# Kernel tuning notes

Hardware: AMD Instinct MI355X
Metric: run time of the kernel (lower is better)

The kernel has to match this reference:

```python
import jax, jax.numpy as jnp
import numpy as np

N_NODES = 100000
D = 128


def setup_inputs() -> dict:
    key = jax.random.key(0)
    ks = jax.random.split(key, 6)
    x = jax.random.normal(ks[0], (N_NODES, 300), dtype=jnp.float32)
    n_id = jnp.arange(N_NODES, dtype=jnp.int64)
    edge_index = jax.random.randint(ks[1], (2, 1600000), 0, N_NODES, dtype=jnp.int64)
    history = jax.random.randint(ks[2], (4096, 50), 0, N_NODES, dtype=jnp.int64)
    candidates = jax.random.randint(ks[3], (4096, 20), 0, N_NODES, dtype=jnp.int64)
    W_enc = jax.random.normal(ks[4], (300, D), dtype=jnp.float32) * 0.05
    W_gnn = jax.random.normal(ks[5], (D, D), dtype=jnp.float32) * 0.05
    return {"x": x, "n_id": n_id, "edge_index": edge_index,
            "history": history, "candidates": candidates,
            "W_enc": W_enc, "W_gnn": W_gnn}


def reference(x, n_id, edge_index, history, candidates, W_enc, W_gnn):
    N = x.shape[0]
    # news encoder: linear projection of raw node features -> [N, D]
    news_emb = x @ W_enc
    # gnn: mean aggregation over incoming edges, then linear
    src, dst = edge_index[0], edge_index[1]
    agg = jax.ops.segment_sum(news_emb[src], dst, num_segments=N)      # [N, D]
    deg = jax.ops.segment_sum(jnp.ones((src.shape[0], 1), news_emb.dtype), dst,
                              num_segments=N)                          # [N, 1]
    struct_emb = (agg / jnp.maximum(deg, 1.0)) @ W_gnn
    xx = news_emb + struct_emb                                          # [N, D]
    # scatter into dense lookup table (n_id == arange -> max_id == N, static)
    news_lookup = jnp.zeros((N, xx.shape[1]), xx.dtype).at[n_id].set(xx)
    # gather histories / candidates
    history_embs = news_lookup[history]                                 # [B, H, D]
    cand_embs = news_lookup[candidates]                                 # [B, C, D]
    mask = (history != 0).astype(xx.dtype)                              # [B, H]
    sum_embs = jnp.einsum('bhd,bh->bd', history_embs, mask)
    num_read = jnp.clip(mask.sum(axis=1, keepdims=True), 1e-9, None)
    user_vec = sum_embs / num_read                                      # [B, D]
    scores = jnp.einsum('bcd,bd->bc', cand_embs, user_vec)              # [B, C]
    return scores
```

## Files before the change

### kernel.cpp

```cpp
#include <hip/hip_runtime.h>

#define NN 100000
#define DD 128
#define KE 300
#define NE 1600000
#define NB 4096
#define HL 50
#define CL 20

#define NBUCK 1563
#define SLOT  1280
#define PBLK  250
#define EPB   6400
#define EPT   25
#define EBLK  1563
#define ENCB  512

#define WTE_N 40960
#define WTG_N 16384
#define PREPB ((WTE_N + WTG_N + 255) / 256)

typedef unsigned short ushort_t;
typedef unsigned char uchar_t;
using bf16x8 = __attribute__((ext_vector_type(8))) short;
using f32x4  = __attribute__((ext_vector_type(4))) float;
using v2f    = __attribute__((ext_vector_type(2))) float;

union U4B { uint4 u; bf16x8 b; unsigned a[4]; };

__device__ __forceinline__ ushort_t f2bf(float f) {
    unsigned u = __float_as_uint(f);
    unsigned r = u + 0x7FFF + ((u >> 16) & 1);
    return (ushort_t)(r >> 16);
}
__device__ __forceinline__ float bf2f(unsigned s) {
    return __uint_as_float(s << 16);
}
__device__ __forceinline__ bf16x8 pack8(float4 a, float4 b) {
    U4B r;
    r.a[0] = (unsigned)f2bf(a.x) | ((unsigned)f2bf(a.y) << 16);
    r.a[1] = (unsigned)f2bf(a.z) | ((unsigned)f2bf(a.w) << 16);
    r.a[2] = (unsigned)f2bf(b.x) | ((unsigned)f2bf(b.y) << 16);
    r.a[3] = (unsigned)f2bf(b.z) | ((unsigned)f2bf(b.w) << 16);
    return r.b;
}

__device__ __forceinline__ bf16x8 loadA8m(const float* __restrict__ x,
                                          int row, int col, bool rowok) {
    float v[8];
#pragma unroll
    for (int j = 0; j < 8; ++j) {
        int c = col + j;
        v[j] = (rowok && c < KE) ? x[(long long)row * KE + c] : 0.f;
    }
    return pack8(make_float4(v[0], v[1], v[2], v[3]),
                 make_float4(v[4], v[5], v[6], v[7]));
}

__global__ __launch_bounds__(256) void k_prep(const int* __restrict__ ei,
                                              unsigned* __restrict__ gcur,
                                              unsigned* __restrict__ pairs,
                                              const float* __restrict__ We,
                                              const float* __restrict__ Wg,
                                              ushort_t* __restrict__ wte,
                                              ushort_t* __restrict__ wtg) {
    __shared__ unsigned sh[NBUCK], sb[NBUCK], sc[NBUCK];
    const int tid = threadIdx.x;

    if (blockIdx.x < PBLK) {
        const int eb = blockIdx.x * EPB;
        for (int i = tid; i < NBUCK; i += 256) sh[i] = 0;
        __syncthreads();

        unsigned val[EPT], bk[EPT];
#pragma unroll
        for (int l = 0; l < EPT; ++l) {
            int e = eb + l * 256 + tid;
            unsigned src = (unsigned)ei[e];
            unsigned dst = (unsigned)ei[NE + e];
            val[l] = (src << 6) | (dst & 63u);
            bk[l] = dst >> 6;
            atomicAdd(&sh[bk[l]], 1u);
        }
        __syncthreads();

        for (int i = tid; i < NBUCK; i += 256) {
            unsigned h = sh[i];
            sb[i] = (unsigned)i * SLOT + (h ? atomicAdd(&gcur[i], h) : 0u);
            sc[i] = 0;
        }
        __syncthreads();

#pragma unroll
        for (int l = 0; l < EPT; ++l) {
            unsigned b = bk[l];
            unsigned pos = sb[b] + atomicAdd(&sc[b], 1u);
            if (pos < (b + 1u) * SLOT) pairs[pos] = val[l];
        }
        return;
    }

    int i = (blockIdx.x - PBLK) * 256 + tid;
    if (i < WTE_N) {
        int j = i & 7, lane = (i >> 3) & 63, cf = (i >> 9) & 7, ch = i >> 12;
        int k = ch * 32 + (lane >> 4) * 8 + j;
        int n = cf * 16 + (lane & 15);
        wte[i] = f2bf((k < KE) ? We[k * DD + n] : 0.f);
    } else if (i < WTE_N + WTG_N) {
        int t = i - WTE_N;
        int j = t & 7, lane = (t >> 3) & 63, cf = (t >> 9) & 7, ks = t >> 12;
        int k = ks * 32 + (lane >> 4) * 8 + j;
        int n = cf * 16 + (lane & 15);
        wtg[t] = f2bf(Wg[k * DD + n]);
    }
}

__global__ __launch_bounds__(256, 1) void enc_mfma(const float* __restrict__ x,
                                                   const ushort_t* __restrict__ wtF,
                                                   ushort_t* __restrict__ news,
                                                   uchar_t* __restrict__ nf8) {
    __shared__ uchar_t f8s[64 * DD];
    const int tid = threadIdx.x;
    const int w = tid >> 6, lane = tid & 63;
    const int hl = lane & 15, kg = lane >> 4;

    bf16x8 B[10][8];
#pragma unroll
    for (int c = 0; c < 10; ++c)
#pragma unroll
        for (int cf = 0; cf < 8; ++cf)
            B[c][cf] = *(const bf16x8*)&wtF[(c * 8 + cf) * 512 + lane * 8];

    for (int tile = blockIdx.x; tile < EBLK; tile += gridDim.x) {
        const int row0 = tile * 64 + w * 16;
        const int r0 = row0 + hl;
        const bool ok0 = r0 < NN;
        const float* xr = &x[(long long)r0 * KE + kg * 8];
        const float4 fz = make_float4(0.f, 0.f, 0.f, 0.f);

        float4 ra[9][2];
        if (ok0) {
#pragma unroll
            for (int c = 0; c < 9; ++c) {
                const float4* p = (const float4*)(xr + c * 32);
                ra[c][0] = p[0];
                ra[c][1] = p[1];
            }
        } else {
#pragma unroll
            for (int c = 0; c < 9; ++c) { ra[c][0] = fz; ra[c][1] = fz; }
        }
        bf16x8 a9 = loadA8m(x, r0, 288 + kg * 8, ok0);

        f32x4 acc[8];
#pragma unroll
        for (int j = 0; j < 8; ++j) acc[j] = (f32x4)0.f;

#pragma unroll
        for (int c = 0; c < 9; ++c) {
            bf16x8 a = pack8(ra[c][0], ra[c][1]);
#pragma unroll
            for (int cf = 0; cf < 8; ++cf)
                acc[cf] = __builtin_amdgcn_mfma_f32_16x16x32_bf16(a, B[c][cf], acc[cf], 0, 0, 0);
        }
#pragma unroll
        for (int cf = 0; cf < 8; ++cf)
            acc[cf] = __builtin_amdgcn_mfma_f32_16x16x32_bf16(a9, B[9][cf], acc[cf], 0, 0, 0);

#pragma unroll
        for (int cf = 0; cf < 8; ++cf)
#pragma unroll
            for (int j = 0; j < 4; ++j) {
                int lr = w * 16 + kg * 4 + j;
                int grow = tile * 64 + lr;
                int gcol = cf * 16 + hl;
                if (grow < NN)
                    news[(long long)grow * DD + gcol] = f2bf(acc[cf][j]);
                int p = __builtin_amdgcn_cvt_pk_fp8_f32(acc[cf][j], 0.f, 0, false);
                f8s[lr * DD + gcol] = (uchar_t)(p & 0xFF);
            }
        __syncthreads();
        {
            int r = tid >> 2, boff = (tid & 3) * 32;
            int grow = tile * 64 + r;
            if (grow < NN) {
                const uint4* s = (const uint4*)&f8s[r * DD + boff];
                uint4* d = (uint4*)&nf8[(long long)grow * DD + boff];
                d[0] = s[0];
                d[1] = s[1];
            }
        }
        __syncthreads();
    }
}

__global__ __launch_bounds__(512) void k_baggnn(const unsigned* __restrict__ gcur,
                                                const unsigned* __restrict__ pairs,
                                                const uchar_t* __restrict__ nf8,
                                                const ushort_t* __restrict__ news,
                                                const ushort_t* __restrict__ wtF,
                                                ushort_t* __restrict__ xxb) {
    __shared__ unsigned srcs[SLOT];
    __shared__ unsigned hist[64], base[64], cur[64];
    __shared__ ushort_t aggs[64 * DD];
    const int tid = threadIdx.x;
    const int b = blockIdx.x;
    int cnt = (int)gcur[b];
    if (cnt > SLOT) cnt = SLOT;

    if (tid < 64) hist[tid] = 0;
    __syncthreads();
    for (int i = tid; i < cnt; i += 512)
        atomicAdd(&hist[pairs[b * SLOT + i] & 63u], 1u);
    __syncthreads();

    if (tid < 64) {
        unsigned h = hist[tid], v = h;
#pragma unroll
        for (int off = 1; off < 64; off <<= 1) {
            unsigned n = __shfl_up(v, off);
            if (tid >= off) v += n;
        }
        base[tid] = v - h;
        cur[tid]  = v - h;
    }
    __syncthreads();

    for (int i = tid; i < cnt; i += 512) {
        unsigned v = pairs[b * SLOT + i];
        srcs[atomicAdd(&cur[v & 63u], 1u)] = v >> 6;
    }
    __syncthreads();

    const int w = tid >> 6, lane = tid & 63;
    const int e = lane >> 4, l = lane & 15;
    for (int d = w; d < 64; d += 8) {
        int gd = b * 64 + d;
        if (gd >= NN) break;
        int s0 = (int)base[d], c = (int)hist[d];
        float acc[8];
#pragma unroll
        for (int j = 0; j < 8; ++j) acc[j] = 0.f;

        uint2 v = make_uint2(0u, 0u);
        if (e < c)
            v = *(const uint2*)&nf8[(long long)srcs[s0 + e] * DD + l * 8];
        for (int i = 4; i < c; i += 4) {
            uint2 vn = make_uint2(0u, 0u);
            int ii = i + e;
            if (ii < c)
                vn = *(const uint2*)&nf8[(long long)srcs[s0 + ii] * DD + l * 8];
            v2f d0 = __builtin_amdgcn_cvt_pk_f32_fp8((int)v.x, false);
            v2f d1 = __builtin_amdgcn_cvt_pk_f32_fp8((int)v.x, true);
            acc[0] += d0[0]; acc[1] += d0[1]; acc[2] += d1[0]; acc[3] += d1[1];
            d0 = __builtin_amdgcn_cvt_pk_f32_fp8((int)v.y, false);
            d1 = __builtin_amdgcn_cvt_pk_f32_fp8((int)v.y, true);
            acc[4] += d0[0]; acc[5] += d0[1]; acc[6] += d1[0]; acc[7] += d1[1];
            v = vn;
        }
        {
            v2f d0 = __builtin_amdgcn_cvt_pk_f32_fp8((int)v.x, false);
            v2f d1 = __builtin_amdgcn_cvt_pk_f32_fp8((int)v.x, true);
            acc[0] += d0[0]; acc[1] += d0[1]; acc[2] += d1[0]; acc[3] += d1[1];
            d0 = __builtin_amdgcn_cvt_pk_f32_fp8((int)v.y, false);
            d1 = __builtin_amdgcn_cvt_pk_f32_fp8((int)v.y, true);
            acc[4] += d0[0]; acc[5] += d0[1]; acc[6] += d1[0]; acc[7] += d1[1];
        }

#pragma unroll
        for (int j = 0; j < 8; ++j) {
            acc[j] += __shfl_xor(acc[j], 16);
            acc[j] += __shfl_xor(acc[j], 32);
        }
        if (e == 0) {
            uint4 o;
            o.x = (unsigned)f2bf(acc[0]) | ((unsigned)f2bf(acc[1]) << 16);
            o.y = (unsigned)f2bf(acc[2]) | ((unsigned)f2bf(acc[3]) << 16);
            o.z = (unsigned)f2bf(acc[4]) | ((unsigned)f2bf(acc[5]) << 16);
            o.w = (unsigned)f2bf(acc[6]) | ((unsigned)f2bf(acc[7]) << 16);
            *(uint4*)&aggs[d * DD + (l ^ (d & 15)) * 8] = o;
        }
    }
    __syncthreads();

    const int hl = lane & 15, kg = lane >> 4;
    const int rw = (w & 3) * 16;
    const int cfb = (w >> 2) * 4;
    U4B a[4];
#pragma unroll
    for (int ks = 0; ks < 4; ++ks)
        a[ks].u = *(const uint4*)&aggs[(rw + hl) * DD + ((ks * 4 + kg) ^ hl) * 8];

    f32x4 acc[4];
#pragma unroll
    for (int j = 0; j < 4; ++j) acc[j] = (f32x4)0.f;

#pragma unroll
    for (int ks = 0; ks < 4; ++ks) {
        const ushort_t* bp = &wtF[(ks * 8 + cfb) * 512 + lane * 8];
#pragma unroll
        for (int cf = 0; cf < 4; ++cf) {
            bf16x8 bfr = *(const bf16x8*)&bp[cf * 512];
            acc[cf] = __builtin_amdgcn_mfma_f32_16x16x32_bf16(a[ks].b, bfr, acc[cf], 0, 0, 0);
        }
    }

#pragma unroll
    for (int j = 0; j < 4; ++j) {
        int lr = rw + kg * 4 + j;
        int grow = b * 64 + lr;
        if (grow < NN) {
            float s = 1.f / fmaxf((float)hist[lr], 1.f);
#pragma unroll
            for (int cf = 0; cf < 4; ++cf) {
                int gcol = (cfb + cf) * 16 + hl;
                float nv = bf2f((unsigned)news[(long long)grow * DD + gcol]);
                xxb[(long long)grow * DD + gcol] = f2bf(nv + acc[cf][j] * s);
            }
        }
    }
}

__global__ __launch_bounds__(128) void k_user(const int* __restrict__ hist,
                                              const int* __restrict__ cand,
                                              const ushort_t* __restrict__ xxb,
                                              float* __restrict__ out) {
    __shared__ float part[2][128];
    __shared__ float cnts[2];
    __shared__ float uvs[128];
    const int b = blockIdx.x, t = threadIdx.x;
    const int w = t >> 6, lane = t & 63;

    float s0 = 0.f, s1 = 0.f, cnt = 0.f;
    for (int h = w; h < HL; h += 2) {
        int id = hist[b * HL + h];
        if (id != 0) {
            unsigned v = *(const unsigned*)&xxb[(long long)id * DD + lane * 2];
            s0 += bf2f(v & 0xFFFFu);
            s1 += bf2f(v >> 16);
            cnt += 1.f;
        }
    }
    part[w][lane * 2]     = s0;
    part[w][lane * 2 + 1] = s1;
    if (lane == 0) cnts[w] = cnt;
    __syncthreads();

    float inv = 1.f / fmaxf(cnts[0] + cnts[1], 1e-9f);
    uvs[t] = (part[0][t] + part[1][t]) * inv;
    __syncthreads();

    float2 uvp = *(const float2*)&uvs[lane * 2];
    for (int c = w; c < CL; c += 2) {
        int id = cand[b * CL + c];
        unsigned v = *(const unsigned*)&xxb[(long long)id * DD + lane * 2];
        float p = uvp.x * bf2f(v & 0xFFFFu) + uvp.y * bf2f(v >> 16);
#pragma unroll
        for (int off = 32; off >= 1; off >>= 1) p += __shfl_xor(p, off);
        if (lane == 0) out[b * CL + c] = p;
    }
}

extern "C" void kernel_launch(void* const* d_in, const int* in_sizes, int n_in,
                              void* d_out, int out_size, void* d_ws, size_t ws_size,
                              hipStream_t stream) {
    const float* x    = (const float*)d_in[0];
    const int*   ei   = (const int*)d_in[2];
    const int*   hist = (const int*)d_in[3];
    const int*   cand = (const int*)d_in[4];
    const float* Wenc = (const float*)d_in[5];
    const float* Wgnn = (const float*)d_in[6];
    float* out = (float*)d_out;

    ushort_t* news_bf = (ushort_t*)d_ws;
    ushort_t* xx_bf   = news_bf + (size_t)NN * DD;
    ushort_t* wt_enc  = xx_bf + (size_t)NN * DD;
    ushort_t* wt_gnn  = wt_enc + WTE_N;
    uchar_t*  news_f8 = (uchar_t*)(wt_gnn + WTG_N);
    unsigned* gcur    = (unsigned*)(news_f8 + (size_t)NN * DD);
    unsigned* pairs   = gcur + NBUCK;

    hipMemsetAsync(gcur, 0, NBUCK * sizeof(unsigned), stream);

    k_prep<<<PBLK + PREPB, 256, 0, stream>>>(ei, gcur, pairs, Wenc, Wgnn, wt_enc, wt_gnn);
    enc_mfma<<<ENCB, 256, 0, stream>>>(x, wt_enc, news_bf, news_f8);
    k_baggnn<<<NBUCK, 512, 0, stream>>>(gcur, pairs, news_f8, news_bf, wt_gnn, xx_bf);
    k_user<<<NB, 128, 0, stream>>>(hist, cand, xx_bf, out);
}
```

Measured before the change: 155.7 us.

## Move fp8 conversion out of encoder into separate kernel, split x loads

Removes the fp8 shared-memory staging and both block barriers from the encoder MFMA loop, so the encoder only writes bf16. A new kernel then reads the bf16 embeddings back and converts them to fp8 with packed converts. The encoder's x loads are also split into two batches so the first five chunks are packed to bf16 before the rest are loaded, which should lower register pressure. The cost is an extra launch plus an extra read of 25.6 MB of bf16 and a second write pass. The fp8 values now come from bf16-rounded results rather than fp32 accumulators, so rounding differs slightly.

```diff
diff --git a/kernel.cpp b/kernel.cpp
--- a/kernel.cpp
+++ b/kernel.cpp
@@ -117,9 +117,7 @@
 
 __global__ __launch_bounds__(256, 1) void enc_mfma(const float* __restrict__ x,
                                                    const ushort_t* __restrict__ wtF,
-                                                   ushort_t* __restrict__ news,
-                                                   uchar_t* __restrict__ nf8) {
-    __shared__ uchar_t f8s[64 * DD];
+                                                   ushort_t* __restrict__ news) {
     const int tid = threadIdx.x;
     const int w = tid >> 6, lane = tid & 63;
     const int hl = lane & 15, kg = lane >> 4;
@@ -138,17 +136,33 @@
         const float* xr = &x[(long long)r0 * KE + kg * 8];
         const float4 fz = make_float4(0.f, 0.f, 0.f, 0.f);
 
-        float4 ra[9][2];
+        float4 ra0[5][2];
         if (ok0) {
 #pragma unroll
-            for (int c = 0; c < 9; ++c) {
+            for (int c = 0; c < 5; ++c) {
                 const float4* p = (const float4*)(xr + c * 32);
-                ra[c][0] = p[0];
-                ra[c][1] = p[1];
+                ra0[c][0] = p[0];
+                ra0[c][1] = p[1];
             }
         } else {
 #pragma unroll
-            for (int c = 0; c < 9; ++c) { ra[c][0] = fz; ra[c][1] = fz; }
+            for (int c = 0; c < 5; ++c) { ra0[c][0] = fz; ra0[c][1] = fz; }
+        }
+        bf16x8 A0[5];
+#pragma unroll
+        for (int c = 0; c < 5; ++c) A0[c] = pack8(ra0[c][0], ra0[c][1]);
+
+        float4 ra1[4][2];
+        if (ok0) {
+#pragma unroll
+            for (int c = 0; c < 4; ++c) {
+                const float4* p = (const float4*)(xr + (5 + c) * 32);
+                ra1[c][0] = p[0];
+                ra1[c][1] = p[1];
+            }
+        } else {
+#pragma unroll
+            for (int c = 0; c < 4; ++c) { ra1[c][0] = fz; ra1[c][1] = fz; }
         }
         bf16x8 a9 = loadA8m(x, r0, 288 + kg * 8, ok0);
 
@@ -157,11 +171,17 @@
         for (int j = 0; j < 8; ++j) acc[j] = (f32x4)0.f;
 
 #pragma unroll
-        for (int c = 0; c < 9; ++c) {
-            bf16x8 a = pack8(ra[c][0], ra[c][1]);
+        for (int c = 0; c < 5; ++c)
 #pragma unroll
             for (int cf = 0; cf < 8; ++cf)
-                acc[cf] = __builtin_amdgcn_mfma_f32_16x16x32_bf16(a, B[c][cf], acc[cf], 0, 0, 0);
+                acc[cf] = __builtin_amdgcn_mfma_f32_16x16x32_bf16(A0[c], B[c][cf], acc[cf], 0, 0, 0);
+
+#pragma unroll
+        for (int c = 0; c < 4; ++c) {
+            bf16x8 a = pack8(ra1[c][0], ra1[c][1]);
+#pragma unroll
+            for (int cf = 0; cf < 8; ++cf)
+                acc[cf] = __builtin_amdgcn_mfma_f32_16x16x32_bf16(a, B[5 + c][cf], acc[cf], 0, 0, 0);
         }
 #pragma unroll
         for (int cf = 0; cf < 8; ++cf)
@@ -171,27 +191,28 @@
         for (int cf = 0; cf < 8; ++cf)
 #pragma unroll
             for (int j = 0; j < 4; ++j) {
-                int lr = w * 16 + kg * 4 + j;
-                int grow = tile * 64 + lr;
+                int grow = row0 + kg * 4 + j;
                 int gcol = cf * 16 + hl;
                 if (grow < NN)
                     news[(long long)grow * DD + gcol] = f2bf(acc[cf][j]);
-                int p = __builtin_amdgcn_cvt_pk_fp8_f32(acc[cf][j], 0.f, 0, false);
-                f8s[lr * DD + gcol] = (uchar_t)(p & 0xFF);
             }
-        __syncthreads();
-        {
-            int r = tid >> 2, boff = (tid & 3) * 32;
-            int grow = tile * 64 + r;
-            if (grow < NN) {
-                const uint4* s = (const uint4*)&f8s[r * DD + boff];
-                uint4* d = (uint4*)&nf8[(long long)grow * DD + boff];
-                d[0] = s[0];
-                d[1] = s[1];
-            }
-        }
-        __syncthreads();
-    }
+    }
+}
+
+__global__ __launch_bounds__(256) void k_cvt8(const ushort_t* __restrict__ nb,
+                                              uchar_t* __restrict__ n8) {
+    long long i = (long long)blockIdx.x * 256 + threadIdx.x;
+    uint4 v = *(const uint4*)&nb[i * 8];
+    float f[8];
+    f[0] = bf2f(v.x & 0xFFFFu); f[1] = bf2f(v.x >> 16);
+    f[2] = bf2f(v.y & 0xFFFFu); f[3] = bf2f(v.y >> 16);
+    f[4] = bf2f(v.z & 0xFFFFu); f[5] = bf2f(v.z >> 16);
+    f[6] = bf2f(v.w & 0xFFFFu); f[7] = bf2f(v.w >> 16);
+    int p0 = __builtin_amdgcn_cvt_pk_fp8_f32(f[0], f[1], 0, false);
+    p0     = __builtin_amdgcn_cvt_pk_fp8_f32(f[2], f[3], p0, true);
+    int p1 = __builtin_amdgcn_cvt_pk_fp8_f32(f[4], f[5], 0, false);
+    p1     = __builtin_amdgcn_cvt_pk_fp8_f32(f[6], f[7], p1, true);
+    *(uint2*)&n8[i * 8] = make_uint2((unsigned)p0, (unsigned)p1);
 }
 
 __global__ __launch_bounds__(512) void k_baggnn(const unsigned* __restrict__ gcur,
@@ -383,7 +404,8 @@
     hipMemsetAsync(gcur, 0, NBUCK * sizeof(unsigned), stream);
 
     k_prep<<<PBLK + PREPB, 256, 0, stream>>>(ei, gcur, pairs, Wenc, Wgnn, wt_enc, wt_gnn);
-    enc_mfma<<<ENCB, 256, 0, stream>>>(x, wt_enc, news_bf, news_f8);
+    enc_mfma<<<ENCB, 256, 0, stream>>>(x, wt_enc, news_bf);
+    k_cvt8<<<(NN * DD / 8 + 255) / 256, 256, 0, stream>>>(news_bf, news_f8);
     k_baggnn<<<NBUCK, 512, 0, stream>>>(gcur, pairs, news_f8, news_bf, wt_gnn, xx_bf);
     k_user<<<NB, 128, 0, stream>>>(hist, cand, xx_bf, out);
 }
```

Measured after the change: 159.4 us. 1.02x slower.
